# Kernel optimization log

Measured on AMD Instinct MI355X. Metric: run time of the kernel, lower is better.

## Reference

```python
import jax, jax.numpy as jnp
import numpy as np

B, T, D, H, NB, K, CDIM, CTX = 8, 4096, 3, 128, 6, 20, 128, 7


def setup_inputs() -> dict:
    key = jax.random.key(0)
    ks = jax.random.split(key, 16)
    s = 0.05
    inp = {
        'p': jax.random.normal(ks[0], (B, T, D), jnp.float32),
        'W_pos': jax.random.normal(ks[1], (D, H), jnp.float32) * s,
        'b_pos': jnp.zeros((H,), jnp.float32),
        # ResnetBlockFC(2H -> H): fc_0(2H,H), fc_1(H,H), shortcut(2H,H, no bias)
        'blk_W0': jax.random.normal(ks[2], (NB, 2 * H, H), jnp.float32) * s,
        'blk_b0': jnp.zeros((NB, H), jnp.float32),
        'blk_W1': jax.random.normal(ks[3], (NB, H, H), jnp.float32) * s,
        'blk_b1': jnp.zeros((NB, H), jnp.float32),
        'blk_Ws': jax.random.normal(ks[4], (NB, 2 * H, H), jnp.float32) * s,
        # Attention: score MLP on context (dim 7 -> 1), output proj (H -> H)
        'att_Wc': jax.random.normal(ks[5], (NB, CTX, 1), jnp.float32) * s,
        'att_bc': jnp.zeros((NB, 1), jnp.float32),
        'att_Wo': jax.random.normal(ks[6], (NB, H, H), jnp.float32) * s,
        'att_bo': jnp.zeros((NB, H), jnp.float32),
        'W_c': jax.random.normal(ks[7], (H, CDIM), jnp.float32) * s,
        'b_c': jnp.zeros((CDIM,), jnp.float32),
    }
    return inp


def _knn(p):
    # squared pairwise distances [B,T,T], top-K smallest
    sq = jnp.sum(p * p, axis=-1)  # [B,T]
    d2 = sq[:, :, None] + sq[:, None, :] - 2.0 * jnp.einsum('btd,bsd->bts', p, p)
    neg, idx = jax.lax.top_k(-d2, K)            # idx: [B,T,K]
    dis = jnp.sqrt(jnp.maximum(-neg, 1e-12))    # euclidean distance [B,T,K]
    return dis, idx


def _gather(c, idx):
    # c: [B,T,h], idx: [B,T,K] -> [B,T,K,h]  (vectorized pool_local)
    return jax.vmap(lambda ci, ii: ci[ii])(c, idx)


def _resnet_block(x, W0, b0, W1, b1, Ws):
    # occupancy-networks ResnetBlockFC: shortcut(x) + fc_1(relu(fc_0(relu(x))))
    h = jnp.maximum(x, 0.0) @ W0 + b0
    dx = jnp.maximum(h, 0.0) @ W1 + b1
    return x @ Ws + dx


def reference(p, W_pos, b_pos, blk_W0, blk_b0, blk_W1, blk_b1, blk_Ws,
              att_Wc, att_bc, att_Wo, att_bo, W_c, b_c):
    dis, idx = _knn(p)
    pooled_points = _gather(p, idx)                                   # [B,T,K,3]
    p_rep = jnp.broadcast_to(p[:, :, None, :], (B, T, K, D))
    context = jnp.concatenate([dis[..., None], pooled_points, p_rep], axis=-1)  # [B,T,K,7]

    net = p @ W_pos + b_pos                                           # [B,T,H]
    last_net = jnp.zeros_like(net)
    for i in range(NB):
        pooled = _gather(net, idx)                                    # [B,T,K,H]
        # attention over the K neighbors, weights from context
        scores = context @ att_Wc[i] + att_bc[i]                      # [B,T,K,1]
        w = jax.nn.softmax(scores, axis=2)
        att = jnp.sum(w * pooled, axis=2) @ att_Wo[i] + att_bo[i]     # [B,T,H]
        x = jnp.concatenate([net, att], axis=2)                       # [B,T,2H]
        net = _resnet_block(x, blk_W0[i], blk_b0[i], blk_W1[i], blk_b1[i], blk_Ws[i])
        net = net + last_net
        last_net = net
    return net @ W_c + b_c                                            # [B,T,c_dim]
```

## Files before the change

kernel.cpp:

```cpp
#include <hip/hip_runtime.h>
#include <hip/hip_bf16.h>
#include <math.h>

#define BB 8
#define TT 4096
#define HHD 128
#define NBK 6
#define KNN 20
#define BT (BB*TT)

typedef __attribute__((ext_vector_type(8))) short bf16x8;
typedef __attribute__((ext_vector_type(4))) float f32x4;

__device__ __forceinline__ float b2f(unsigned short u){
  return __uint_as_float(((unsigned int)u) << 16);
}
__device__ __forceinline__ unsigned short f2b(float f){
  unsigned int x = __float_as_uint(f);
  unsigned int r = (x + 0x7fffu + ((x >> 16) & 1u)) >> 16;
  return (unsigned short)r;
}
__device__ __forceinline__ float ldp(const void* base, int i, int f32m){
  return f32m ? ((const float*)base)[i] : b2f(((const unsigned short*)base)[i]);
}
__device__ __forceinline__ float lo2f(unsigned int u){ return __uint_as_float(u << 16); }
__device__ __forceinline__ float hi2f(unsigned int u){ return __uint_as_float(u & 0xffff0000u); }
__device__ __forceinline__ unsigned int relu2(unsigned int u){
  unsigned int s = u & 0x80008000u;
  unsigned int m = s | (s - (s >> 15));
  return u & ~m;
}
__device__ __forceinline__ bf16x8 relu8(bf16x8 x){
  union { bf16x8 v; unsigned int u[4]; } t; t.v = x;
  t.u[0] = relu2(t.u[0]); t.u[1] = relu2(t.u[1]);
  t.u[2] = relu2(t.u[2]); t.u[3] = relu2(t.u[3]);
  return t.v;
}
__device__ __forceinline__ unsigned int splitpk(float v){
  unsigned short h = f2b(v);
  float hv = b2f(h);
  unsigned short l = f2b(v - hv);
  return (unsigned int)h | ((unsigned int)l << 16);
}

__global__ void k_detect(const unsigned short* __restrict__ wpos_raw, int* __restrict__ flag){
  int lane = threadIdx.x;
  int cnt = 0;
  for (int i = lane; i < 384; i += 64) {
    unsigned int e = (wpos_raw[i] >> 7) & 0xFFu;
    if (e >= 0x90u) cnt++;
  }
  #pragma unroll
  for (int off = 32; off > 0; off >>= 1) cnt += __shfl_down(cnt, off);
  if (lane == 0) *flag = (cnt > 10) ? 1 : 0;
}

__global__ __launch_bounds__(256) void k_prep_points(const void* __restrict__ p,
                                                     const int* __restrict__ flagp,
                                                     float4* __restrict__ pf4){
  int r = blockIdx.x*256 + threadIdx.x;
  if (r >= BT) return;
  int f32m = *flagp;
  float x = ldp(p, r*3+0, f32m), y = ldp(p, r*3+1, f32m), z = ldp(p, r*3+2, f32m);
  float sq = __fadd_rn(__fadd_rn(__fmul_rn(x,x), __fmul_rn(y,y)), __fmul_rn(z,z));
  pf4[r] = make_float4(x, y, z, sq);
}

__global__ __launch_bounds__(256) void k_net0(const float4* __restrict__ pf4,
                                              const void* __restrict__ Wpos,
                                              const void* __restrict__ bpos,
                                              const int* __restrict__ flagp,
                                              unsigned short* __restrict__ netA){
  int t = blockIdx.x*256 + threadIdx.x;
  int f32m = *flagp;
  int c = t & 127, r = t >> 7;
  float4 q = pf4[r];
  float v = ldp(bpos, c, f32m);
  v = fmaf(q.x, ldp(Wpos, c,       f32m), v);
  v = fmaf(q.y, ldp(Wpos, 128 + c, f32m), v);
  v = fmaf(q.z, ldp(Wpos, 256 + c, f32m), v);
  netA[t] = f2b(v);
}

__global__ __launch_bounds__(256) void k_transpose(const void* __restrict__ W0,
                                                   const void* __restrict__ W1,
                                                   const void* __restrict__ Ws,
                                                   const void* __restrict__ Wo,
                                                   const void* __restrict__ Wc,
                                                   const int* __restrict__ flagp,
                                                   unsigned short* __restrict__ wT){
  int t = blockIdx.x*256 + threadIdx.x;
  int f32m = *flagp;
  if (t < 196608) {
    int i = t >> 15; int rem = t & 32767; int n = rem >> 8; int k = rem & 255;
    wT[t] = f2b(ldp(W0, i*32768 + k*128 + n, f32m));
  } else if (t < 294912) {
    int u = t - 196608; int i = u >> 14; int rem = u & 16383; int n = rem >> 7; int k = rem & 127;
    wT[t] = f2b(ldp(W1, i*16384 + k*128 + n, f32m));
  } else if (t < 491520) {
    int u = t - 294912; int i = u >> 15; int rem = u & 32767; int n = rem >> 8; int k = rem & 255;
    wT[t] = f2b(ldp(Ws, i*32768 + k*128 + n, f32m));
  } else if (t < 589824) {
    int u = t - 491520; int i = u >> 14; int rem = u & 16383; int n = rem >> 7; int k = rem & 127;
    wT[t] = f2b(ldp(Wo, i*16384 + k*128 + n, f32m));
  } else if (t < 606208) {
    int u = t - 589824; int n = u >> 7; int k = u & 127;
    wT[t] = f2b(ldp(Wc, k*128 + n, f32m));
  }
}

#define INS(act, dv, iv) do { bool A_ = (act); float D_ = (dv); int I_ = (iv);        \
  _Pragma("unroll")                                                                    \
  for (int j = 19; j >= 1; --j) {                                                      \
    bool cj = A_ && (D_ < ld[j]); bool cm = A_ && (D_ < ld[j-1]);                      \
    ld[j] = cj ? (cm ? ld[j-1] : D_) : ld[j];                                          \
    li[j] = cj ? (cm ? li[j-1] : I_) : li[j];                                          \
  }                                                                                    \
  { bool c0 = A_ && (D_ < ld[0]); ld[0] = c0 ? D_ : ld[0]; li[0] = c0 ? I_ : li[0]; } \
} while(0)

#define KCAP   20
#define MARGIN 0.02f

#define KNN_FLUSH() do {                                                               \
  int mc_ = cnt;                                                                       \
  _Pragma("unroll")                                                                    \
  for (int o_ = 32; o_ > 0; o_ >>= 1) { int t_ = __shfl_xor(mc_, o_); mc_ = mc_ > t_ ? mc_ : t_; } \
  _Pragma("unroll 1")                                                                  \
  for (int u_ = 0; u_ < mc_; ++u_) {                                                   \
    float2 e_ = stk[u_*256 + tid];                                                     \
    bool act_ = u_ < cnt;                                                              \
    int piv_ = __float_as_int(e_.y);                                                   \
    float4 pp_ = tilef4[act_ ? (piv_ - ch*512) : 0];                                   \
    float dot_ = __fadd_rn(__fadd_rn(__fmul_rn(q.x,pp_.x), __fmul_rn(q.y,pp_.y)),      \
                           __fmul_rn(q.z,pp_.z));                                      \
    float d2e_ = __fsub_rn(__fadd_rn(q.w, pp_.w), __fmul_rn(2.0f, dot_));              \
    INS(act_, d2e_, piv_);                                                             \
  }                                                                                    \
  cnt = 0;                                                                             \
  atomicMin(&sthr[qlocal], __float_as_uint(fmaxf(ld[19], 0.0f)));                      \
  threshP = fminf(ld[19], __uint_as_float(sthr[qlocal])) + MARGIN;                     \
} while(0)

__global__ __launch_bounds__(256) void k_knn(const float4* __restrict__ pf4,
                                             const void* __restrict__ Wc,
                                             const void* __restrict__ bc,
                                             const int* __restrict__ flagp,
                                             unsigned short* __restrict__ idx16,
                                             unsigned short* __restrict__ wsoftb){
  __shared__ __align__(16) char smem[57344];
  __shared__ unsigned int sthr[64];
  float4* tilef4 = (float4*)smem;
  uint4*  tilesp = (uint4*)(smem + 8192);
  float2* stk    = (float2*)(smem + 16384);
  float*  lsd    = (float*)(smem + 16384);
  int*    lsi    = (int*)(smem + 36864);

  int tid  = threadIdx.x;
  int wv   = tid >> 6, lane = tid & 63;
  int cq   = lane & 15;
  int kg   = lane >> 4;
  int qlocal = wv*16 + cq;
  int b    = blockIdx.x >> 6;
  int f32m = *flagp;
  float4 q = pf4[blockIdx.x*64 + qlocal];

  if (tid < 64) sthr[tid] = 0x7F7FFFFFu;

  union FRU { bf16x8 v; unsigned int u[4]; };
  FRU bfr;
  {
    float e = (kg == 0) ? -2.0f*q.x : -2.0f*q.z;
    unsigned int ehl = splitpk(e);
    unsigned int eh = ehl & 0xffffu, el = ehl >> 16;
    float f = (kg == 0) ? -2.0f*q.y : q.w;
    unsigned int fhl = splitpk(f);
    unsigned int fh = fhl & 0xffffu, fl = fhl >> 16;
    unsigned int v0 = eh | (eh << 16);
    unsigned int v1 = el | (el << 16);
    unsigned int v2 = (kg == 0) ? (fh | (fh << 16)) : 0x3F803F80u;
    unsigned int v3 = (kg == 0) ? (fl | (fl << 16)) : fhl;
    if (kg >= 2) { v0 = 0; v1 = 0; v2 = 0; v3 = 0; }
    bfr.u[0] = v0; bfr.u[1] = v1; bfr.u[2] = v2; bfr.u[3] = v3;
  }
  const f32x4 zf = {0.f, 0.f, 0.f, 0.f};

  float ld[20]; int li[20];
  #pragma unroll
  for (int j = 0; j < 20; ++j) { ld[j] = 3.0e38f; li[j] = 0; }
  float threshP = 3.0e38f;
  int cnt = 0;

  for (int ch = 0; ch < 8; ++ch) {
    __syncthreads();
    {
      const float4* src = pf4 + (b << 12) + ch*512;
      float4 a0 = src[tid], a1 = src[tid + 256];
      tilef4[tid]       = a0;
      tilef4[tid + 256] = a1;
      tilesp[tid]       = make_uint4(splitpk(a0.x), splitpk(a0.y), splitpk(a0.z), splitpk(a0.w));
      tilesp[tid + 256] = make_uint4(splitpk(a1.x), splitpk(a1.y), splitpk(a1.z), splitpk(a1.w));
    }
    __syncthreads();
    threshP = fminf(ld[19], __uint_as_float(sthr[qlocal])) + MARGIN;
    #pragma unroll 4
    for (int g = 0; g < 32; ++g) {
      uint4 s = tilesp[g*16 + cq];
      unsigned int u0 = (kg == 0) ? s.x : s.z;
      unsigned int u2 = (kg == 0) ? s.y : s.w;
      unsigned int u3 = (kg == 0) ? u2 : 0x3F803F80u;
      if (kg >= 2) { u0 = 0; u2 = 0; u3 = 0; }
      FRU afr; afr.u[0] = u0; afr.u[1] = u0; afr.u[2] = u2; afr.u[3] = u3;
      f32x4 dd = __builtin_amdgcn_mfma_f32_16x16x32_bf16(afr.v, bfr.v, zf, 0, 0, 0);
      int pbase = ch*512 + g*16 + kg*4;
      #pragma unroll
      for (int r = 0; r < 4; ++r) {
        if (dd[r] < threshP) {
          stk[cnt*256 + tid] = make_float2(dd[r], __int_as_float(pbase + r));
          cnt++;
        }
      }
      if (__ballot(cnt >= KCAP-3)) KNN_FLUSH();
    }
    if (__ballot(cnt > 0)) KNN_FLUSH();
  }

  __syncthreads();
  #pragma unroll
  for (int j = 0; j < 20; ++j) { lsd[tid*20 + j] = ld[j]; lsi[tid*20 + j] = li[j]; }
  __syncthreads();

  if (tid < 64) {
    int w2 = tid >> 4, c2 = tid & 15;
    int base = w2*64 + c2;
    int p0 = base*20, p1 = (base+16)*20, p2 = (base+32)*20, p3 = (base+48)*20;
    int i0 = 0, i1 = 0, i2 = 0, i3 = 0;
    int rq = blockIdx.x*64 + tid;
    float4 qq = pf4[rq];
    float dis[20]; int outi[20];
    #pragma unroll
    for (int o = 0; o < 20; ++o) {
      float d0 = lsd[p0+i0], d1 = lsd[p1+i1], d2v = lsd[p2+i2], d3 = lsd[p3+i3];
      int   j0 = lsi[p0+i0], j1 = lsi[p1+i1], j2  = lsi[p2+i2], j3 = lsi[p3+i3];
      float bd = d0; int bi = j0; int sel = 0;
      if (d1  < bd || (d1  == bd && j1 < bi)) { bd = d1;  bi = j1; sel = 1; }
      if (d2v < bd || (d2v == bd && j2 < bi)) { bd = d2v; bi = j2; sel = 2; }
      if (d3  < bd || (d3  == bd && j3 < bi)) { bd = d3;  bi = j3; sel = 3; }
      i0 += (sel==0); i1 += (sel==1); i2 += (sel==2); i3 += (sel==3);
      dis[o] = sqrtf(fmaxf(bd, 1e-12f));
      outi[o] = bi;
    }
    float nx[20], ny[20], nz[20];
    #pragma unroll
    for (int k = 0; k < 20; ++k) {
      idx16[rq*20 + k] = (unsigned short)outi[k];
      float4 pp = pf4[(b << 12) + outi[k]];
      nx[k] = pp.x; ny[k] = pp.y; nz[k] = pp.z;
    }
    for (int i = 0; i < NBK; ++i) {
      float w0 = ldp(Wc,i*7+0,f32m), w1 = ldp(Wc,i*7+1,f32m), w2 = ldp(Wc,i*7+2,f32m);
      float w3 = ldp(Wc,i*7+3,f32m), w4 = ldp(Wc,i*7+4,f32m), w5 = ldp(Wc,i*7+5,f32m);
      float w6 = ldp(Wc,i*7+6,f32m);
      float bci = ldp(bc,i,f32m);
      float s[20]; float mx = -3.0e38f;
      #pragma unroll
      for (int k = 0; k < 20; ++k) {
        float v = bci;
        v = fmaf(dis[k], w0, v);
        v = fmaf(nx[k], w1, v); v = fmaf(ny[k], w2, v); v = fmaf(nz[k], w3, v);
        v = fmaf(qq.x, w4, v);  v = fmaf(qq.y, w5, v);  v = fmaf(qq.z, w6, v);
        s[k] = v; mx = fmaxf(mx, v);
      }
      float sum = 0.f;
      #pragma unroll
      for (int k = 0; k < 20; ++k) { float e = __expf(s[k] - mx); s[k] = e; sum += e; }
      float inv = 1.0f / sum;
      #pragma unroll
      for (int k = 0; k < 20; ++k) wsoftb[(rq*6 + i)*20 + k] = f2b(s[k]*inv);
    }
  }
}

__global__ __launch_bounds__(128) void k_block(const unsigned short* __restrict__ netIn,
                                               unsigned short* __restrict__ netOut,
                                               const unsigned short* __restrict__ idx16,
                                               const unsigned short* __restrict__ wsoftb,
                                               const unsigned short* __restrict__ wT,
                                               const void* __restrict__ b0s,
                                               const void* __restrict__ b1s,
                                               const void* __restrict__ bos,
                                               const int* __restrict__ flagp,
                                               int iblk, int hasResid){
  __shared__ unsigned short ldsA[16*136];
  __shared__ unsigned short ldsH[16*136];
  int tid = threadIdx.x;
  int f32m = *flagp;
  int c = tid >> 6, lane = tid & 63;
  int b  = blockIdx.x & 7;
  int r0 = (b << 12) + ((blockIdx.x >> 3) << 4);
  const unsigned short* W0T = wT + iblk*32768;
  const unsigned short* W1T = wT + 196608 + iblk*16384;
  const unsigned short* WsT = wT + 294912 + iblk*32768;
  const unsigned short* WoT = wT + 491520 + iblk*16384;
  int m = lane & 15, qd = lane >> 4;

  {
    int r = lane >> 2, cg = lane & 3;
    int grow = r0 + r;
    int cbase = c*64 + cg*16;
    const unsigned int* ip = (const unsigned int*)(idx16 + grow*20);
    const unsigned int* wp = (const unsigned int*)(wsoftb + (grow*6 + iblk)*20);
    unsigned int iv[10], wv[10];
    #pragma unroll
    for (int j = 0; j < 10; ++j) iv[j] = ip[j];
    #pragma unroll
    for (int j = 0; j < 10; ++j) wv[j] = wp[j];
    float acc[16];
    #pragma unroll
    for (int j = 0; j < 16; ++j) acc[j] = 0.f;
    #pragma unroll
    for (int k = 0; k < 20; ++k) {
      unsigned int pair = iv[k >> 1];
      int nb = (int)((k & 1) ? (pair >> 16) : pair) & 4095;
      unsigned int wpair = wv[k >> 1];
      float wk = (k & 1) ? hi2f(wpair) : lo2f(wpair);
      const uint4* np_ = (const uint4*)(netIn + ((b << 12) + nb)*128 + cbase);
      #pragma unroll
      for (int u = 0; u < 2; ++u) {
        uint4 uu = np_[u];
        acc[u*8+0] = fmaf(wk, lo2f(uu.x), acc[u*8+0]);
        acc[u*8+1] = fmaf(wk, hi2f(uu.x), acc[u*8+1]);
        acc[u*8+2] = fmaf(wk, lo2f(uu.y), acc[u*8+2]);
        acc[u*8+3] = fmaf(wk, hi2f(uu.y), acc[u*8+3]);
        acc[u*8+4] = fmaf(wk, lo2f(uu.z), acc[u*8+4]);
        acc[u*8+5] = fmaf(wk, hi2f(uu.z), acc[u*8+5]);
        acc[u*8+6] = fmaf(wk, lo2f(uu.w), acc[u*8+6]);
        acc[u*8+7] = fmaf(wk, hi2f(uu.w), acc[u*8+7]);
      }
    }
    #pragma unroll
    for (int j = 0; j < 8; ++j) {
      unsigned int pr = ((unsigned int)f2b(acc[2*j+1]) << 16) | (unsigned int)f2b(acc[2*j]);
      *(unsigned int*)(ldsH + r*136 + cbase + 2*j) = pr;
    }
  }
  __syncthreads();

  {
    bf16x8 asf[4];
    #pragma unroll
    for (int ks = 0; ks < 4; ++ks)
      asf[ks] = *(const bf16x8*)(ldsH + m*136 + ks*32 + qd*8);
    f32x4 acc2[4];
    #pragma unroll
    for (int i = 0; i < 4; ++i) { f32x4 z = {0.f,0.f,0.f,0.f}; acc2[i] = z; }
    #pragma unroll
    for (int i = 0; i < 4; ++i) {
      int cti = c*4 + i;
      const unsigned short* bp = WoT + (cti*16 + m)*128 + qd*8;
      #pragma unroll
      for (int ks = 0; ks < 4; ++ks)
        acc2[i] = __builtin_amdgcn_mfma_f32_16x16x32_bf16(asf[ks], *(const bf16x8*)(bp + ks*32), acc2[i], 0, 0, 0);
    }
    #pragma unroll
    for (int i = 0; i < 4; ++i) {
      int col = (c*4 + i)*16 + m;
      float bo = ldp(bos, iblk*128 + col, f32m);
      #pragma unroll
      for (int rr = 0; rr < 4; ++rr)
        ldsA[(qd*4 + rr)*136 + col] = f2b(acc2[i][rr] + bo);
    }
  }
  __syncthreads();

  bf16x8 nf[4], af[4];
  {
    const unsigned short* nrow = netIn + (r0 + m)*128;
    #pragma unroll
    for (int ks = 0; ks < 4; ++ks) nf[ks] = *(const bf16x8*)(nrow + ks*32 + qd*8);
    #pragma unroll
    for (int ks = 0; ks < 4; ++ks) af[ks] = *(const bf16x8*)(ldsA + m*136 + ks*32 + qd*8);
    bf16x8 rnf[4], raf[4];
    #pragma unroll
    for (int ks = 0; ks < 4; ++ks) { rnf[ks] = relu8(nf[ks]); raf[ks] = relu8(af[ks]); }
    f32x4 acc3[4];
    #pragma unroll
    for (int i = 0; i < 4; ++i) { f32x4 z = {0.f,0.f,0.f,0.f}; acc3[i] = z; }
    #pragma unroll
    for (int i = 0; i < 4; ++i) {
      int cti = c*4 + i;
      const unsigned short* bp = W0T + (cti*16 + m)*256 + qd*8;
      #pragma unroll
      for (int ks = 0; ks < 4; ++ks)
        acc3[i] = __builtin_amdgcn_mfma_f32_16x16x32_bf16(rnf[ks], *(const bf16x8*)(bp + ks*32), acc3[i], 0, 0, 0);
      #pragma unroll
      for (int ks = 0; ks < 4; ++ks)
        acc3[i] = __builtin_amdgcn_mfma_f32_16x16x32_bf16(raf[ks], *(const bf16x8*)(bp + 128 + ks*32), acc3[i], 0, 0, 0);
    }
    #pragma unroll
    for (int i = 0; i < 4; ++i) {
      int col = (c*4 + i)*16 + m;
      float b0v = ldp(b0s, iblk*128 + col, f32m);
      #pragma unroll
      for (int rr = 0; rr < 4; ++rr)
        ldsH[(qd*4 + rr)*136 + col] = f2b(fmaxf(acc3[i][rr] + b0v, 0.f));
    }
  }
  __syncthreads();

  {
    bf16x8 hf[4];
    #pragma unroll
    for (int ks = 0; ks < 4; ++ks) hf[ks] = *(const bf16x8*)(ldsH + m*136 + ks*32 + qd*8);
    f32x4 acc4[4];
    #pragma unroll
    for (int i = 0; i < 4; ++i) { f32x4 z = {0.f,0.f,0.f,0.f}; acc4[i] = z; }
    #pragma unroll
    for (int i = 0; i < 4; ++i) {
      int cti = c*4 + i;
      const unsigned short* bp1 = W1T + (cti*16 + m)*128 + qd*8;
      #pragma unroll
      for (int ks = 0; ks < 4; ++ks)
        acc4[i] = __builtin_amdgcn_mfma_f32_16x16x32_bf16(hf[ks], *(const bf16x8*)(bp1 + ks*32), acc4[i], 0, 0, 0);
      const unsigned short* bps = WsT + (cti*16 + m)*256 + qd*8;
      #pragma unroll
      for (int ks = 0; ks < 4; ++ks)
        acc4[i] = __builtin_amdgcn_mfma_f32_16x16x32_bf16(nf[ks], *(const bf16x8*)(bps + ks*32), acc4[i], 0, 0, 0);
      #pragma unroll
      for (int ks = 0; ks < 4; ++ks)
        acc4[i] = __builtin_amdgcn_mfma_f32_16x16x32_bf16(af[ks], *(const bf16x8*)(bps + 128 + ks*32), acc4[i], 0, 0, 0);
    }
    #pragma unroll
    for (int i = 0; i < 4; ++i) {
      int col = (c*4 + i)*16 + m;
      float b1v = ldp(b1s, iblk*128 + col, f32m);
      #pragma unroll
      for (int rr = 0; rr < 4; ++rr) {
        int grow2 = r0 + qd*4 + rr;
        float v = acc4[i][rr] + b1v;
        if (hasResid) v += b2f(netIn[grow2*128 + col]);
        netOut[grow2*128 + col] = f2b(v);
      }
    }
  }
}

__global__ __launch_bounds__(256) void k_final(const unsigned short* __restrict__ netIn,
                                               const unsigned short* __restrict__ WcT,
                                               const void* __restrict__ bcv,
                                               const int* __restrict__ flagp,
                                               void* __restrict__ out){
  int tid = threadIdx.x; int w = tid >> 6, lane = tid & 63;
  int f32m = *flagp;
  int t = w >> 1, c = w & 1;
  int r0 = blockIdx.x*32 + t*16;
  int m = lane & 15, qd = lane >> 4;
  bf16x8 nf[4];
  #pragma unroll
  for (int ks = 0; ks < 4; ++ks)
    nf[ks] = *(const bf16x8*)(netIn + (r0 + m)*128 + ks*32 + qd*8);
  f32x4 acc[4];
  #pragma unroll
  for (int i = 0; i < 4; ++i) { f32x4 z = {0.f,0.f,0.f,0.f}; acc[i] = z; }
  #pragma unroll
  for (int i = 0; i < 4; ++i) {
    int cti = c*4 + i;
    const unsigned short* bp = WcT + (cti*16 + m)*128 + qd*8;
    #pragma unroll
    for (int ks = 0; ks < 4; ++ks)
      acc[i] = __builtin_amdgcn_mfma_f32_16x16x32_bf16(nf[ks], *(const bf16x8*)(bp + ks*32), acc[i], 0, 0, 0);
  }
  if (f32m) {
    float* o = (float*)out;
    #pragma unroll
    for (int i = 0; i < 4; ++i) {
      int col = (c*4 + i)*16 + m;
      float bcf = ldp(bcv, col, 1);
      #pragma unroll
      for (int rr = 0; rr < 4; ++rr)
        o[(r0 + qd*4 + rr)*128 + col] = acc[i][rr] + bcf;
    }
  } else {
    unsigned short* o = (unsigned short*)out;
    #pragma unroll
    for (int i = 0; i < 4; ++i) {
      int col = (c*4 + i)*16 + m;
      float bcf = ldp(bcv, col, 0);
      #pragma unroll
      for (int rr = 0; rr < 4; ++rr)
        o[(r0 + qd*4 + rr)*128 + col] = f2b(acc[i][rr] + bcf);
    }
  }
}

extern "C" void kernel_launch(void* const* d_in, const int* in_sizes, int n_in,
                              void* d_out, int out_size, void* d_ws, size_t ws_size,
                              hipStream_t stream){
  const void* p    = d_in[0];
  const void* Wpos = d_in[1];
  const void* bpos = d_in[2];
  const void* W0   = d_in[3];
  const void* b0   = d_in[4];
  const void* W1   = d_in[5];
  const void* b1   = d_in[6];
  const void* Ws   = d_in[7];
  const void* Wc_  = d_in[8];
  const void* bc_  = d_in[9];
  const void* Wo   = d_in[10];
  const void* bo   = d_in[11];
  const void* WC   = d_in[12];
  const void* bC   = d_in[13];

  char* ws = (char*)d_ws;
  int*            flag   = (int*)(ws + 0);
  float4*         pf4    = (float4*)(ws + 256);
  unsigned short* idx16  = (unsigned short*)(ws + 524544);
  unsigned short* wsoftb = (unsigned short*)(ws + 1835264);
  unsigned short* netA   = (unsigned short*)(ws + 9699584);
  unsigned short* wT     = (unsigned short*)(ws + 18088192);

  k_detect     <<<dim3(1),     dim3(64),  0, stream>>>((const unsigned short*)Wpos, flag);
  k_prep_points<<<dim3(128),   dim3(256), 0, stream>>>(p, flag, pf4);
  k_net0       <<<dim3(16384), dim3(256), 0, stream>>>(pf4, Wpos, bpos, flag, netA);
  k_transpose  <<<dim3(2368),  dim3(256), 0, stream>>>(W0, W1, Ws, Wo, WC, flag, wT);
  k_knn        <<<dim3(512),   dim3(256), 0, stream>>>(pf4, Wc_, bc_, flag, idx16, wsoftb);

  unsigned short* a   = netA;
  unsigned short* bpt = (unsigned short*)d_out;
  for (int i = 0; i < 6; ++i) {
    k_block<<<dim3(2048), dim3(128), 0, stream>>>(a, bpt, idx16, wsoftb, wT,
                                                  b0, b1, bo, flag, i, (i > 0) ? 1 : 0);
    unsigned short* t = a; a = bpt; bpt = t;
  }
  k_final<<<dim3(1024), dim3(256), 0, stream>>>(a, wT + 589824, bC, flag, d_out);
}
```

Measured before the change: 700.4 us.

## Seed KNN threshold from an upper-bound prepass and compute exact distances at candidate time

Adds a prepass over the first 320 points of the first tile: for each query it takes the max over 20 groups of each group's minimum approximate distance, an upper bound on the 20th-nearest distance, and seeds the shared per-query threshold with it. This lets the main loop reject most candidates from the start instead of filling the stack early. The exact fp32 distance is now computed when a candidate is pushed, while its tile is still in LDS, so flushes can be deferred past tile boundaries and happen once at the end. The gather loop's unroll is reduced to 4, which trades register pressure against instruction-level parallelism.

```diff
diff --git a/kernel.cpp b/kernel.cpp
--- a/kernel.cpp
+++ b/kernel.cpp
@@ -129,13 +129,7 @@
   _Pragma("unroll 1")                                                                  \
   for (int u_ = 0; u_ < mc_; ++u_) {                                                   \
     float2 e_ = stk[u_*256 + tid];                                                     \
-    bool act_ = u_ < cnt;                                                              \
-    int piv_ = __float_as_int(e_.y);                                                   \
-    float4 pp_ = tilef4[act_ ? (piv_ - ch*512) : 0];                                   \
-    float dot_ = __fadd_rn(__fadd_rn(__fmul_rn(q.x,pp_.x), __fmul_rn(q.y,pp_.y)),      \
-                           __fmul_rn(q.z,pp_.z));                                      \
-    float d2e_ = __fsub_rn(__fadd_rn(q.w, pp_.w), __fmul_rn(2.0f, dot_));              \
-    INS(act_, d2e_, piv_);                                                             \
+    INS(u_ < cnt, e_.x, __float_as_int(e_.y));                                         \
   }                                                                                    \
   cnt = 0;                                                                             \
   atomicMin(&sthr[qlocal], __float_as_uint(fmaxf(ld[19], 0.0f)));                      \
@@ -191,17 +185,45 @@
   float threshP = 3.0e38f;
   int cnt = 0;
 
+  {
+    const float4* src = pf4 + (b << 12);
+    float4 a0 = src[tid], a1 = src[tid + 256];
+    tilef4[tid]       = a0;
+    tilef4[tid + 256] = a1;
+    tilesp[tid]       = make_uint4(splitpk(a0.x), splitpk(a0.y), splitpk(a0.z), splitpk(a0.w));
+    tilesp[tid + 256] = make_uint4(splitpk(a1.x), splitpk(a1.y), splitpk(a1.z), splitpk(a1.w));
+  }
+  __syncthreads();
+
+  {
+    float smax = -3.0e38f;
+    #pragma unroll 4
+    for (int g = 0; g < 20; ++g) {
+      uint4 s = tilesp[g*16 + cq];
+      unsigned int u0 = (kg == 0) ? s.x : s.z;
+      unsigned int u2 = (kg == 0) ? s.y : s.w;
+      unsigned int u3 = (kg == 0) ? u2 : 0x3F803F80u;
+      if (kg >= 2) { u0 = 0; u2 = 0; u3 = 0; }
+      FRU afr; afr.u[0] = u0; afr.u[1] = u0; afr.u[2] = u2; afr.u[3] = u3;
+      f32x4 dd = __builtin_amdgcn_mfma_f32_16x16x32_bf16(afr.v, bfr.v, zf, 0, 0, 0);
+      float gmin = fminf(fminf(dd[0], dd[1]), fminf(dd[2], dd[3]));
+      smax = fmaxf(smax, gmin);
+    }
+    atomicMin(&sthr[qlocal], __float_as_uint(fmaxf(smax + MARGIN, 0.0f)));
+  }
+  __syncthreads();
+
   for (int ch = 0; ch < 8; ++ch) {
-    __syncthreads();
-    {
+    if (ch > 0) {
+      __syncthreads();
       const float4* src = pf4 + (b << 12) + ch*512;
       float4 a0 = src[tid], a1 = src[tid + 256];
       tilef4[tid]       = a0;
       tilef4[tid + 256] = a1;
       tilesp[tid]       = make_uint4(splitpk(a0.x), splitpk(a0.y), splitpk(a0.z), splitpk(a0.w));
       tilesp[tid + 256] = make_uint4(splitpk(a1.x), splitpk(a1.y), splitpk(a1.z), splitpk(a1.w));
-    }
-    __syncthreads();
+      __syncthreads();
+    }
     threshP = fminf(ld[19], __uint_as_float(sthr[qlocal])) + MARGIN;
     #pragma unroll 4
     for (int g = 0; g < 32; ++g) {
@@ -212,18 +234,23 @@
       if (kg >= 2) { u0 = 0; u2 = 0; u3 = 0; }
       FRU afr; afr.u[0] = u0; afr.u[1] = u0; afr.u[2] = u2; afr.u[3] = u3;
       f32x4 dd = __builtin_amdgcn_mfma_f32_16x16x32_bf16(afr.v, bfr.v, zf, 0, 0, 0);
-      int pbase = ch*512 + g*16 + kg*4;
+      int lbase = g*16 + kg*4;
+      int pbase = ch*512 + lbase;
       #pragma unroll
       for (int r = 0; r < 4; ++r) {
         if (dd[r] < threshP) {
-          stk[cnt*256 + tid] = make_float2(dd[r], __int_as_float(pbase + r));
+          float4 pp = tilef4[lbase + r];
+          float dot = __fadd_rn(__fadd_rn(__fmul_rn(q.x,pp.x), __fmul_rn(q.y,pp.y)),
+                                __fmul_rn(q.z,pp.z));
+          float d2e = __fsub_rn(__fadd_rn(q.w, pp.w), __fmul_rn(2.0f, dot));
+          stk[cnt*256 + tid] = make_float2(d2e, __int_as_float(pbase + r));
           cnt++;
         }
       }
       if (__ballot(cnt >= KCAP-3)) KNN_FLUSH();
     }
-    if (__ballot(cnt > 0)) KNN_FLUSH();
-  }
+  }
+  if (__ballot(cnt > 0)) KNN_FLUSH();
 
   __syncthreads();
   #pragma unroll
@@ -318,7 +345,7 @@
     float acc[16];
     #pragma unroll
     for (int j = 0; j < 16; ++j) acc[j] = 0.f;
-    #pragma unroll
+    #pragma unroll 4
     for (int k = 0; k < 20; ++k) {
       unsigned int pair = iv[k >> 1];
       int nb = (int)((k & 1) ? (pair >> 16) : pair) & 4095;
```

Result: faster. 637.5 us (-9.0%).

## Double k_block threads, split columns across four waves, stage output through LDS

Applied to the files above, without the earlier changes.

k_block now runs 256 threads (four waves) per 16-row tile instead of 128, and each wave computes two 16-column MFMA tiles instead of four. The neighbor gather moves to one thread per 8 columns with a partially unrolled loop, which cuts register pressure so launch_bounds(256,8) can raise occupancy. The final result goes through a float LDS buffer so the residual add and the store become coalesced 16-byte vector accesses. The cost is one extra barrier and more LDS per block, and the net and activation fragments are now reloaded rather than kept in registers.

```diff
diff --git a/kernel.cpp b/kernel.cpp
--- a/kernel.cpp
+++ b/kernel.cpp
@@ -281,18 +281,19 @@
   }
 }
 
-__global__ __launch_bounds__(128) void k_block(const unsigned short* __restrict__ netIn,
-                                               unsigned short* __restrict__ netOut,
-                                               const unsigned short* __restrict__ idx16,
-                                               const unsigned short* __restrict__ wsoftb,
-                                               const unsigned short* __restrict__ wT,
-                                               const void* __restrict__ b0s,
-                                               const void* __restrict__ b1s,
-                                               const void* __restrict__ bos,
-                                               const int* __restrict__ flagp,
-                                               int iblk, int hasResid){
+__global__ __launch_bounds__(256, 8) void k_block(const unsigned short* __restrict__ netIn,
+                                                  unsigned short* __restrict__ netOut,
+                                                  const unsigned short* __restrict__ idx16,
+                                                  const unsigned short* __restrict__ wsoftb,
+                                                  const unsigned short* __restrict__ wT,
+                                                  const void* __restrict__ b0s,
+                                                  const void* __restrict__ b1s,
+                                                  const void* __restrict__ bos,
+                                                  const int* __restrict__ flagp,
+                                                  int iblk, int hasResid){
   __shared__ unsigned short ldsA[16*136];
   __shared__ unsigned short ldsH[16*136];
+  __shared__ float ldsF[16*132];
   int tid = threadIdx.x;
   int f32m = *flagp;
   int c = tid >> 6, lane = tid & 63;
@@ -305,41 +306,44 @@
   int m = lane & 15, qd = lane >> 4;
 
   {
-    int r = lane >> 2, cg = lane & 3;
+    int r = tid >> 4, cg = tid & 15;
     int grow = r0 + r;
-    int cbase = c*64 + cg*16;
+    int cbase = cg*8;
     const unsigned int* ip = (const unsigned int*)(idx16 + grow*20);
     const unsigned int* wp = (const unsigned int*)(wsoftb + (grow*6 + iblk)*20);
-    unsigned int iv[10], wv[10];
-    #pragma unroll
-    for (int j = 0; j < 10; ++j) iv[j] = ip[j];
-    #pragma unroll
-    for (int j = 0; j < 10; ++j) wv[j] = wp[j];
-    float acc[16];
-    #pragma unroll
-    for (int j = 0; j < 16; ++j) acc[j] = 0.f;
-    #pragma unroll
-    for (int k = 0; k < 20; ++k) {
-      unsigned int pair = iv[k >> 1];
-      int nb = (int)((k & 1) ? (pair >> 16) : pair) & 4095;
-      unsigned int wpair = wv[k >> 1];
-      float wk = (k & 1) ? hi2f(wpair) : lo2f(wpair);
-      const uint4* np_ = (const uint4*)(netIn + ((b << 12) + nb)*128 + cbase);
-      #pragma unroll
-      for (int u = 0; u < 2; ++u) {
-        uint4 uu = np_[u];
-        acc[u*8+0] = fmaf(wk, lo2f(uu.x), acc[u*8+0]);
-        acc[u*8+1] = fmaf(wk, hi2f(uu.x), acc[u*8+1]);
-        acc[u*8+2] = fmaf(wk, lo2f(uu.y), acc[u*8+2]);
-        acc[u*8+3] = fmaf(wk, hi2f(uu.y), acc[u*8+3]);
-        acc[u*8+4] = fmaf(wk, lo2f(uu.z), acc[u*8+4]);
-        acc[u*8+5] = fmaf(wk, hi2f(uu.z), acc[u*8+5]);
-        acc[u*8+6] = fmaf(wk, lo2f(uu.w), acc[u*8+6]);
-        acc[u*8+7] = fmaf(wk, hi2f(uu.w), acc[u*8+7]);
-      }
-    }
-    #pragma unroll
-    for (int j = 0; j < 8; ++j) {
+    const unsigned short* nbase = netIn + (b << 12)*128 + cbase;
+    float acc[8];
+    #pragma unroll
+    for (int j = 0; j < 8; ++j) acc[j] = 0.f;
+    #pragma unroll 5
+    for (int kk = 0; kk < 10; ++kk) {
+      unsigned int pair  = ip[kk];
+      unsigned int wpair = wp[kk];
+      int nb0 = (int)(pair & 4095u);
+      int nb1 = (int)((pair >> 16) & 4095u);
+      float wk0 = lo2f(wpair);
+      float wk1 = hi2f(wpair);
+      uint4 a0 = *(const uint4*)(nbase + nb0*128);
+      uint4 a1 = *(const uint4*)(nbase + nb1*128);
+      acc[0] = fmaf(wk0, lo2f(a0.x), acc[0]);
+      acc[1] = fmaf(wk0, hi2f(a0.x), acc[1]);
+      acc[2] = fmaf(wk0, lo2f(a0.y), acc[2]);
+      acc[3] = fmaf(wk0, hi2f(a0.y), acc[3]);
+      acc[4] = fmaf(wk0, lo2f(a0.z), acc[4]);
+      acc[5] = fmaf(wk0, hi2f(a0.z), acc[5]);
+      acc[6] = fmaf(wk0, lo2f(a0.w), acc[6]);
+      acc[7] = fmaf(wk0, hi2f(a0.w), acc[7]);
+      acc[0] = fmaf(wk1, lo2f(a1.x), acc[0]);
+      acc[1] = fmaf(wk1, hi2f(a1.x), acc[1]);
+      acc[2] = fmaf(wk1, lo2f(a1.y), acc[2]);
+      acc[3] = fmaf(wk1, hi2f(a1.y), acc[3]);
+      acc[4] = fmaf(wk1, lo2f(a1.z), acc[4]);
+      acc[5] = fmaf(wk1, hi2f(a1.z), acc[5]);
+      acc[6] = fmaf(wk1, lo2f(a1.w), acc[6]);
+      acc[7] = fmaf(wk1, hi2f(a1.w), acc[7]);
+    }
+    #pragma unroll
+    for (int j = 0; j < 4; ++j) {
       unsigned int pr = ((unsigned int)f2b(acc[2*j+1]) << 16) | (unsigned int)f2b(acc[2*j]);
       *(unsigned int*)(ldsH + r*136 + cbase + 2*j) = pr;
     }
@@ -351,20 +355,20 @@
     #pragma unroll
     for (int ks = 0; ks < 4; ++ks)
       asf[ks] = *(const bf16x8*)(ldsH + m*136 + ks*32 + qd*8);
-    f32x4 acc2[4];
-    #pragma unroll
-    for (int i = 0; i < 4; ++i) { f32x4 z = {0.f,0.f,0.f,0.f}; acc2[i] = z; }
-    #pragma unroll
-    for (int i = 0; i < 4; ++i) {
-      int cti = c*4 + i;
+    f32x4 acc2[2];
+    #pragma unroll
+    for (int i = 0; i < 2; ++i) { f32x4 z = {0.f,0.f,0.f,0.f}; acc2[i] = z; }
+    #pragma unroll
+    for (int i = 0; i < 2; ++i) {
+      int cti = c*2 + i;
       const unsigned short* bp = WoT + (cti*16 + m)*128 + qd*8;
       #pragma unroll
       for (int ks = 0; ks < 4; ++ks)
         acc2[i] = __builtin_amdgcn_mfma_f32_16x16x32_bf16(asf[ks], *(const bf16x8*)(bp + ks*32), acc2[i], 0, 0, 0);
     }
     #pragma unroll
-    for (int i = 0; i < 4; ++i) {
-      int col = (c*4 + i)*16 + m;
+    for (int i = 0; i < 2; ++i) {
+      int col = (c*2 + i)*16 + m;
       float bo = ldp(bos, iblk*128 + col, f32m);
       #pragma unroll
       for (int rr = 0; rr < 4; ++rr)
@@ -373,22 +377,19 @@
   }
   __syncthreads();
 
-  bf16x8 nf[4], af[4];
   {
     const unsigned short* nrow = netIn + (r0 + m)*128;
-    #pragma unroll
-    for (int ks = 0; ks < 4; ++ks) nf[ks] = *(const bf16x8*)(nrow + ks*32 + qd*8);
-    #pragma unroll
-    for (int ks = 0; ks < 4; ++ks) af[ks] = *(const bf16x8*)(ldsA + m*136 + ks*32 + qd*8);
     bf16x8 rnf[4], raf[4];
     #pragma unroll
-    for (int ks = 0; ks < 4; ++ks) { rnf[ks] = relu8(nf[ks]); raf[ks] = relu8(af[ks]); }
-    f32x4 acc3[4];
-    #pragma unroll
-    for (int i = 0; i < 4; ++i) { f32x4 z = {0.f,0.f,0.f,0.f}; acc3[i] = z; }
-    #pragma unroll
-    for (int i = 0; i < 4; ++i) {
-      int cti = c*4 + i;
+    for (int ks = 0; ks < 4; ++ks) rnf[ks] = relu8(*(const bf16x8*)(nrow + ks*32 + qd*8));
+    #pragma unroll
+    for (int ks = 0; ks < 4; ++ks) raf[ks] = relu8(*(const bf16x8*)(ldsA + m*136 + ks*32 + qd*8));
+    f32x4 acc3[2];
+    #pragma unroll
+    for (int i = 0; i < 2; ++i) { f32x4 z = {0.f,0.f,0.f,0.f}; acc3[i] = z; }
+    #pragma unroll
+    for (int i = 0; i < 2; ++i) {
+      int cti = c*2 + i;
       const unsigned short* bp = W0T + (cti*16 + m)*256 + qd*8;
       #pragma unroll
       for (int ks = 0; ks < 4; ++ks)
@@ -398,8 +399,8 @@
         acc3[i] = __builtin_amdgcn_mfma_f32_16x16x32_bf16(raf[ks], *(const bf16x8*)(bp + 128 + ks*32), acc3[i], 0, 0, 0);
     }
     #pragma unroll
-    for (int i = 0; i < 4; ++i) {
-      int col = (c*4 + i)*16 + m;
+    for (int i = 0; i < 2; ++i) {
+      int col = (c*2 + i)*16 + m;
       float b0v = ldp(b0s, iblk*128 + col, f32m);
       #pragma unroll
       for (int rr = 0; rr < 4; ++rr)
@@ -409,39 +410,77 @@
   __syncthreads();
 
   {
-    bf16x8 hf[4];
-    #pragma unroll
-    for (int ks = 0; ks < 4; ++ks) hf[ks] = *(const bf16x8*)(ldsH + m*136 + ks*32 + qd*8);
-    f32x4 acc4[4];
-    #pragma unroll
-    for (int i = 0; i < 4; ++i) { f32x4 z = {0.f,0.f,0.f,0.f}; acc4[i] = z; }
-    #pragma unroll
-    for (int i = 0; i < 4; ++i) {
-      int cti = c*4 + i;
-      const unsigned short* bp1 = W1T + (cti*16 + m)*128 + qd*8;
-      #pragma unroll
-      for (int ks = 0; ks < 4; ++ks)
-        acc4[i] = __builtin_amdgcn_mfma_f32_16x16x32_bf16(hf[ks], *(const bf16x8*)(bp1 + ks*32), acc4[i], 0, 0, 0);
-      const unsigned short* bps = WsT + (cti*16 + m)*256 + qd*8;
-      #pragma unroll
-      for (int ks = 0; ks < 4; ++ks)
-        acc4[i] = __builtin_amdgcn_mfma_f32_16x16x32_bf16(nf[ks], *(const bf16x8*)(bps + ks*32), acc4[i], 0, 0, 0);
-      #pragma unroll
-      for (int ks = 0; ks < 4; ++ks)
-        acc4[i] = __builtin_amdgcn_mfma_f32_16x16x32_bf16(af[ks], *(const bf16x8*)(bps + 128 + ks*32), acc4[i], 0, 0, 0);
-    }
-    #pragma unroll
-    for (int i = 0; i < 4; ++i) {
-      int col = (c*4 + i)*16 + m;
+    f32x4 acc4[2];
+    #pragma unroll
+    for (int i = 0; i < 2; ++i) { f32x4 z = {0.f,0.f,0.f,0.f}; acc4[i] = z; }
+    {
+      bf16x8 hf[4];
+      #pragma unroll
+      for (int ks = 0; ks < 4; ++ks) hf[ks] = *(const bf16x8*)(ldsH + m*136 + ks*32 + qd*8);
+      #pragma unroll
+      for (int i = 0; i < 2; ++i) {
+        int cti = c*2 + i;
+        const unsigned short* bp1 = W1T + (cti*16 + m)*128 + qd*8;
+        #pragma unroll
+        for (int ks = 0; ks < 4; ++ks)
+          acc4[i] = __builtin_amdgcn_mfma_f32_16x16x32_bf16(hf[ks], *(const bf16x8*)(bp1 + ks*32), acc4[i], 0, 0, 0);
+      }
+    }
+    {
+      bf16x8 nf[4];
+      const unsigned short* nrow = netIn + (r0 + m)*128;
+      #pragma unroll
+      for (int ks = 0; ks < 4; ++ks) nf[ks] = *(const bf16x8*)(nrow + ks*32 + qd*8);
+      #pragma unroll
+      for (int i = 0; i < 2; ++i) {
+        int cti = c*2 + i;
+        const unsigned short* bps = WsT + (cti*16 + m)*256 + qd*8;
+        #pragma unroll
+        for (int ks = 0; ks < 4; ++ks)
+          acc4[i] = __builtin_amdgcn_mfma_f32_16x16x32_bf16(nf[ks], *(const bf16x8*)(bps + ks*32), acc4[i], 0, 0, 0);
+      }
+    }
+    {
+      bf16x8 af[4];
+      #pragma unroll
+      for (int ks = 0; ks < 4; ++ks) af[ks] = *(const bf16x8*)(ldsA + m*136 + ks*32 + qd*8);
+      #pragma unroll
+      for (int i = 0; i < 2; ++i) {
+        int cti = c*2 + i;
+        const unsigned short* bps = WsT + (cti*16 + m)*256 + qd*8;
+        #pragma unroll
+        for (int ks = 0; ks < 4; ++ks)
+          acc4[i] = __builtin_amdgcn_mfma_f32_16x16x32_bf16(af[ks], *(const bf16x8*)(bps + 128 + ks*32), acc4[i], 0, 0, 0);
+      }
+    }
+    #pragma unroll
+    for (int i = 0; i < 2; ++i) {
+      int col = (c*2 + i)*16 + m;
       float b1v = ldp(b1s, iblk*128 + col, f32m);
       #pragma unroll
-      for (int rr = 0; rr < 4; ++rr) {
-        int grow2 = r0 + qd*4 + rr;
-        float v = acc4[i][rr] + b1v;
-        if (hasResid) v += b2f(netIn[grow2*128 + col]);
-        netOut[grow2*128 + col] = f2b(v);
-      }
-    }
+      for (int rr = 0; rr < 4; ++rr)
+        ldsF[(qd*4 + rr)*132 + col] = acc4[i][rr] + b1v;
+    }
+  }
+  __syncthreads();
+
+  {
+    int row = tid >> 4, cg2 = tid & 15;
+    int grow2 = r0 + row;
+    const float* srcf = ldsF + row*132 + cg2*8;
+    unsigned int outw[4];
+    if (hasResid) {
+      uint4 ra = *(const uint4*)(netIn + grow2*128 + cg2*8);
+      outw[0] = (unsigned int)f2b(srcf[0] + lo2f(ra.x)) | ((unsigned int)f2b(srcf[1] + hi2f(ra.x)) << 16);
+      outw[1] = (unsigned int)f2b(srcf[2] + lo2f(ra.y)) | ((unsigned int)f2b(srcf[3] + hi2f(ra.y)) << 16);
+      outw[2] = (unsigned int)f2b(srcf[4] + lo2f(ra.z)) | ((unsigned int)f2b(srcf[5] + hi2f(ra.z)) << 16);
+      outw[3] = (unsigned int)f2b(srcf[6] + lo2f(ra.w)) | ((unsigned int)f2b(srcf[7] + hi2f(ra.w)) << 16);
+    } else {
+      #pragma unroll
+      for (int j = 0; j < 4; ++j)
+        outw[j] = (unsigned int)f2b(srcf[2*j]) | ((unsigned int)f2b(srcf[2*j+1]) << 16);
+    }
+    *(uint4*)(netOut + grow2*128 + cg2*8) = make_uint4(outw[0], outw[1], outw[2], outw[3]);
   }
 }
 
@@ -528,7 +567,7 @@
   unsigned short* a   = netA;
   unsigned short* bpt = (unsigned short*)d_out;
   for (int i = 0; i < 6; ++i) {
-    k_block<<<dim3(2048), dim3(128), 0, stream>>>(a, bpt, idx16, wsoftb, wT,
+    k_block<<<dim3(2048), dim3(256), 0, stream>>>(a, bpt, idx16, wsoftb, wT,
                                                   b0, b1, bo, flag, i, (i > 0) ? 1 : 0);
     unsigned short* t = a; a = bpt; bpt = t;
   }
```

Result: faster. 640.5 us (-8.5%).
